# Kernel tuning notes

Hardware: AMD Instinct MI355X
Metric: run time of the kernel (lower is better)

The kernel has to match this reference:

```python
import jax, jax.numpy as jnp
import numpy as np

EMBED_DIM = 1024
NUM_HEADS = 16
HEAD_DIM = EMBED_DIM // NUM_HEADS


def setup_inputs() -> dict:
    key = jax.random.key(0)
    ks = jax.random.split(key, 9)
    B, S, D = 4, 2048, EMBED_DIM
    scale = 1.0 / np.sqrt(D)
    inp = {
        "x": jax.random.normal(ks[0], (B, S, D), dtype=jnp.float32),
        "wq": jax.random.normal(ks[1], (D, D), dtype=jnp.float32) * scale,
        "bq": jnp.zeros((D,), dtype=jnp.float32),
        "wk": jax.random.normal(ks[2], (D, D), dtype=jnp.float32) * scale,
        "bk": jnp.zeros((D,), dtype=jnp.float32),
        "wv": jax.random.normal(ks[3], (D, D), dtype=jnp.float32) * scale,
        "bv": jnp.zeros((D,), dtype=jnp.float32),
        "wo": jax.random.normal(ks[4], (D, D), dtype=jnp.float32) * scale,
        "bo": jnp.zeros((D,), dtype=jnp.float32),
    }
    return inp


def reference(x, wq, bq, wk, bk, wv, bv, wo, bo):
    B, S, D = x.shape
    H, Hd = NUM_HEADS, HEAD_DIM

    def split_heads(t):
        # [B, S, D] -> [B, H, S, Hd]
        return t.reshape(B, S, H, Hd).transpose(0, 2, 1, 3)

    q = split_heads(x @ wq.T + bq)
    k = split_heads(x @ wk.T + bk)
    v = split_heads(x @ wv.T + bv)

    scores = jnp.einsum("bhqd,bhkd->bhqk", q, k) / jnp.sqrt(jnp.float32(Hd))
    attn = jax.nn.softmax(scores, axis=-1)
    out = jnp.einsum("bhqk,bhkd->bhqd", attn, v)  # [B, H, S, Hd]
    out = out.transpose(0, 2, 1, 3).reshape(B, S, D)
    return out @ wo.T + bo
```

## Files before the change

### kernel.cpp

```cpp
#include <hip/hip_runtime.h>
#include <hip/hip_bf16.h>
#include <hip/hip_fp16.h>

typedef _Float16 f16;
typedef f16 f16x8 __attribute__((ext_vector_type(8)));
typedef f16 f16x4 __attribute__((ext_vector_type(4)));
typedef f16 f16x2 __attribute__((ext_vector_type(2)));
typedef float f32x4 __attribute__((ext_vector_type(4)));
typedef float f32x16 __attribute__((ext_vector_type(16)));
typedef unsigned int u32x4 __attribute__((ext_vector_type(4)));
typedef unsigned int u32x2 __attribute__((ext_vector_type(2)));

#define MFMA16(a, b, c) __builtin_amdgcn_mfma_f32_16x16x32_f16(a, b, c, 0, 0, 0)
#define MFMA32(a, b, c) __builtin_amdgcn_mfma_f32_32x32x16_f16(a, b, c, 0, 0, 0)

constexpr int BB = 4, SS = 2048, DD = 1024, HH = 16, HDIM = 64;
constexpr int MM = BB * SS;
constexpr float QSCALE = 0.125f * 1.44269504088896340736f;

__device__ __forceinline__ void gl_lds16(const void* g, void* l) {
  __builtin_amdgcn_global_load_lds((const __attribute__((address_space(1))) void*)g,
                                   (__attribute__((address_space(3))) void*)l, 16, 0, 0);
}

__global__ __launch_bounds__(256) void cvt_kernel(const float* __restrict__ in,
                                                  f16* __restrict__ out, int n4) {
  int i = blockIdx.x * 256 + threadIdx.x;
  if (i < n4) {
    f32x4 v = reinterpret_cast<const f32x4*>(in)[i];
    f16x4 o;
    o[0] = (f16)v[0]; o[1] = (f16)v[1]; o[2] = (f16)v[2]; o[3] = (f16)v[3];
    reinterpret_cast<f16x4*>(out)[i] = o;
  }
}

__global__ __launch_bounds__(256) void cvt4_kernel(const float* __restrict__ w0,
                                                   const float* __restrict__ w1,
                                                   const float* __restrict__ w2,
                                                   const float* __restrict__ w3,
                                                   f16* o0, f16* o1, f16* o2, f16* o3) {
  int i = blockIdx.x * 256 + threadIdx.x;
  const float* in; f16* out;
  switch (blockIdx.y) {
    case 0: in = w0; out = o0; break;
    case 1: in = w1; out = o1; break;
    case 2: in = w2; out = o2; break;
    default: in = w3; out = o3; break;
  }
  f32x4 v = reinterpret_cast<const f32x4*>(in)[i];
  f16x4 o;
  o[0] = (f16)v[0]; o[1] = (f16)v[1]; o[2] = (f16)v[2]; o[3] = (f16)v[3];
  reinterpret_cast<f16x4*>(out)[i] = o;
}

__device__ __forceinline__ int swz(int row, int slot) {
  return row * 64 + ((slot ^ (row & 7)) << 3);
}

__global__ __launch_bounds__(256) void qkv_kernel(const f16* __restrict__ A,
                                                  const f16* __restrict__ Wq,
                                                  const f16* __restrict__ Wk,
                                                  const f16* __restrict__ Wv,
                                                  const float* __restrict__ bq,
                                                  const float* __restrict__ bk,
                                                  const float* __restrict__ bv,
                                                  f16* __restrict__ Qo,
                                                  f16* __restrict__ Ko,
                                                  f16* __restrict__ Vo) {
  constexpr int K = 1024;
  __shared__ __align__(16) char smem_raw[128 * 136 * 2];
  f16* As = (f16*)smem_raw;
  f16* Ws = As + 128 * 64;

  const int mat = blockIdx.x >> 3;
  const f16* W = mat == 0 ? Wq : (mat == 1 ? Wk : Wv);
  const float* bias = mat == 0 ? bq : (mat == 1 ? bk : bv);
  const float scale = mat == 0 ? QSCALE : 1.0f;

  const int tid = threadIdx.x;
  const int m0 = blockIdx.y * 128, n0 = (blockIdx.x & 7) * 128;
  const int w = tid >> 6, lane = tid & 63;
  const int wm = (w >> 1) * 64, wn = (w & 1) * 64;
  const int g = lane >> 4, r = lane & 15;
  const int srow = lane >> 3;
  const int sslot = (lane & 7) ^ srow;

  f32x4 acc[4][4] = {};

  for (int k0 = 0; k0 < K; k0 += 64) {
#pragma unroll
    for (int i = 0; i < 4; ++i) {
      int rbase = w * 32 + i * 8;
      gl_lds16(A + (size_t)(m0 + rbase + srow) * K + k0 + sslot * 8, As + rbase * 64);
      gl_lds16(W + (size_t)(n0 + rbase + srow) * K + k0 + sslot * 8, Ws + rbase * 64);
    }
    __syncthreads();

#pragma unroll
    for (int ks = 0; ks < 2; ++ks) {
      f16x8 af[4], bf[4];
#pragma unroll
      for (int i = 0; i < 4; ++i) {
        af[i] = *reinterpret_cast<const f16x8*>(As + swz(wm + i * 16 + r, (ks << 2) | g));
        bf[i] = *reinterpret_cast<const f16x8*>(Ws + swz(wn + i * 16 + r, (ks << 2) | g));
      }
#pragma unroll
      for (int i = 0; i < 4; ++i)
#pragma unroll
        for (int j = 0; j < 4; ++j)
          acc[i][j] = MFMA16(af[i], bf[j], acc[i][j]);
    }
    __syncthreads();
  }

  if (mat < 2) {
    f16* o = mat == 0 ? Qo : Ko;
#pragma unroll
    for (int i = 0; i < 4; ++i)
#pragma unroll
      for (int j = 0; j < 4; ++j)
#pragma unroll
        for (int q = 0; q < 4; ++q) {
          int gm = m0 + wm + i * 16 + g * 4 + q;
          int gn = n0 + wn + j * 16 + r;
          float v = (acc[i][j][q] + bias[gn]) * scale;
          int b = gm >> 11, s = gm & 2047;
          int h = gn >> 6, hd = gn & 63;
          o[(((size_t)(b * HH + h)) * SS + s) * HDIM + hd] = (f16)v;
        }
  } else {
    __syncthreads();
    f16* T = (f16*)smem_raw;
#pragma unroll
    for (int i = 0; i < 4; ++i)
#pragma unroll
      for (int j = 0; j < 4; ++j)
#pragma unroll
        for (int q = 0; q < 4; ++q) {
          int ml = wm + i * 16 + g * 4 + q;
          int nl = wn + j * 16 + r;
          T[nl * 136 + ml] = (f16)(acc[i][j][q] + bias[n0 + nl]);
        }
    __syncthreads();
    const int b = m0 >> 11, sbase = m0 & 2047;
#pragma unroll
    for (int it = 0; it < 8; ++it) {
      int slot = it * 256 + tid;
      int nl = slot >> 4, mc = (slot & 15) * 8;
      u32x4 v = *reinterpret_cast<const u32x4*>(T + nl * 136 + mc);
      int gn = n0 + nl;
      int h = gn >> 6, hd = gn & 63;
      size_t addr = ((size_t)((b * HH + h) * HDIM + hd)) * SS + sbase + mc;
      *reinterpret_cast<u32x4*>(Vo + addr) = v;
    }
  }
}

__global__ __launch_bounds__(256) void oproj_kernel(const f16* __restrict__ A,
                                                    const f16* __restrict__ W,
                                                    const float* __restrict__ bias,
                                                    float* __restrict__ Out) {
  constexpr int K = 1024, N = 1024;
  __shared__ __align__(16) f16 As[128 * 64];
  __shared__ __align__(16) f16 Ws[128 * 64];

  const int tid = threadIdx.x;
  const int m0 = blockIdx.y * 128, n0 = blockIdx.x * 128;
  const int w = tid >> 6, lane = tid & 63;
  const int wm = (w >> 1) * 64, wn = (w & 1) * 64;
  const int g = lane >> 4, r = lane & 15;
  const int srow = lane >> 3;
  const int sslot = (lane & 7) ^ srow;

  f32x4 acc[4][4] = {};

  for (int k0 = 0; k0 < K; k0 += 64) {
#pragma unroll
    for (int i = 0; i < 4; ++i) {
      int rbase = w * 32 + i * 8;
      gl_lds16(A + (size_t)(m0 + rbase + srow) * K + k0 + sslot * 8, As + rbase * 64);
      gl_lds16(W + (size_t)(n0 + rbase + srow) * K + k0 + sslot * 8, Ws + rbase * 64);
    }
    __syncthreads();

#pragma unroll
    for (int ks = 0; ks < 2; ++ks) {
      f16x8 af[4], bf[4];
#pragma unroll
      for (int i = 0; i < 4; ++i) {
        af[i] = *reinterpret_cast<const f16x8*>(As + swz(wm + i * 16 + r, (ks << 2) | g));
        bf[i] = *reinterpret_cast<const f16x8*>(Ws + swz(wn + i * 16 + r, (ks << 2) | g));
      }
#pragma unroll
      for (int i = 0; i < 4; ++i)
#pragma unroll
        for (int j = 0; j < 4; ++j)
          acc[i][j] = MFMA16(af[i], bf[j], acc[i][j]);
    }
    __syncthreads();
  }

#pragma unroll
  for (int i = 0; i < 4; ++i)
#pragma unroll
    for (int j = 0; j < 4; ++j)
#pragma unroll
      for (int q = 0; q < 4; ++q) {
        int gm = m0 + wm + i * 16 + g * 4 + q;
        int gn = n0 + wn + j * 16 + r;
        Out[(size_t)gm * N + gn] = acc[i][j][q] + bias[gn];
      }
}

__global__ __launch_bounds__(256, 4) void attn_kernel(const f16* __restrict__ Q,
                                                      const f16* __restrict__ K,
                                                      const f16* __restrict__ Vt,
                                                      f16* __restrict__ AO) {
  __shared__ __align__(16) f16 Kls[2][64 * 64];
  __shared__ __align__(16) f16 Vls[2][64 * 64];
  __shared__ __align__(16) float Lw[4][32];

  const int tid = threadIdx.x;
  const int w = tid >> 6, lane = tid & 63;
  const int q31 = lane & 31;
  const int h = lane >> 5;
  const int bh = blockIdx.y;
  const int q0 = blockIdx.x * 128;
  const int srow = lane >> 3;
  const int sslot = (lane & 7) ^ srow;

  const f16* Kg = K + (size_t)bh * SS * HDIM;
  const f16* Vg = Vt + (size_t)bh * HDIM * SS;

  const f16* Qg = Q + ((size_t)bh * SS + q0 + w * 32 + q31) * HDIM + 8 * h;
  f16x8 qf[4];
#pragma unroll
  for (int m = 0; m < 4; ++m)
    qf[m] = *reinterpret_cast<const f16x8*>(Qg + 16 * m);

  f32x16 oacc[2] = {};
  float lsum = 0.f;

#pragma unroll
  for (int i = 0; i < 2; ++i) {
    int rbase = w * 16 + i * 8;
    gl_lds16(Kg + (size_t)(rbase + srow) * HDIM + sslot * 8, &Kls[0][rbase * 64]);
    gl_lds16(Vg + (size_t)(rbase + srow) * SS + sslot * 8, &Vls[0][rbase * 64]);
  }
  __syncthreads();

  for (int t = 0; t < SS / 64; ++t) {
    const int cur = t & 1;
    if (t < SS / 64 - 1) {
      const int kt = (t + 1) * 64;
#pragma unroll
      for (int i = 0; i < 2; ++i) {
        int rbase = w * 16 + i * 8;
        gl_lds16(Kg + (size_t)(kt + rbase + srow) * HDIM + sslot * 8, &Kls[cur ^ 1][rbase * 64]);
        gl_lds16(Vg + (size_t)(rbase + srow) * SS + kt + sslot * 8, &Vls[cur ^ 1][rbase * 64]);
      }
    }
    const f16* Kc = &Kls[cur][0];
    const f16* Vc = &Vls[cur][0];

#pragma unroll
    for (int kb = 0; kb < 2; ++kb) {
      f32x16 sacc = {};
      __builtin_amdgcn_s_setprio(1);
#pragma unroll
      for (int m = 0; m < 4; ++m) {
        f16x8 kf = *reinterpret_cast<const f16x8*>(Kc + swz(32 * kb + q31, 2 * m + h));
        sacc = MFMA32(kf, qf[m], sacc);
      }
      __builtin_amdgcn_s_setprio(0);

      unsigned pk[8];
#pragma unroll
      for (int rp = 0; rp < 4; ++rp)
#pragma unroll
        for (int p = 0; p < 2; ++p) {
          float e0 = __builtin_amdgcn_exp2f(sacc[4 * rp + 2 * p]);
          float e1 = __builtin_amdgcn_exp2f(sacc[4 * rp + 2 * p + 1]);
          pk[2 * rp + p] = __builtin_bit_cast(unsigned, __builtin_amdgcn_cvt_pkrtz(e0, e1));
        }

      f16x2 s01 = __builtin_bit_cast(f16x2, pk[0]) + __builtin_bit_cast(f16x2, pk[1]);
      f16x2 s23 = __builtin_bit_cast(f16x2, pk[2]) + __builtin_bit_cast(f16x2, pk[3]);
      f16x2 s45 = __builtin_bit_cast(f16x2, pk[4]) + __builtin_bit_cast(f16x2, pk[5]);
      f16x2 s67 = __builtin_bit_cast(f16x2, pk[6]) + __builtin_bit_cast(f16x2, pk[7]);
      f16x2 st = (s01 + s23) + (s45 + s67);
      lsum += (float)st[0] + (float)st[1];

#pragma unroll
      for (int jl = 0; jl < 2; ++jl) {
        auto s0 = __builtin_amdgcn_permlane32_swap(pk[4 * jl + 0], pk[4 * jl + 2], false, false);
        auto s1 = __builtin_amdgcn_permlane32_swap(pk[4 * jl + 1], pk[4 * jl + 3], false, false);
        u32x4 fw = {(unsigned)s0[0], (unsigned)s1[0], (unsigned)s0[1], (unsigned)s1[1]};
        f16x8 pa = __builtin_bit_cast(f16x8, fw);
        const int j = 2 * kb + jl;
        __builtin_amdgcn_s_setprio(1);
#pragma unroll
        for (int vb = 0; vb < 2; ++vb) {
          f16x8 vbf = *reinterpret_cast<const f16x8*>(Vc + swz(32 * vb + q31, 2 * j + h));
          oacc[vb] = MFMA32(pa, vbf, oacc[vb]);
        }
        __builtin_amdgcn_s_setprio(0);
      }
    }
    __syncthreads();
  }

  lsum += __shfl_xor(lsum, 32, 64);
  if (h == 0) Lw[w][q31] = 1.0f / lsum;

  f32x4 li[4];
#pragma unroll
  for (int rq = 0; rq < 4; ++rq)
    li[rq] = *reinterpret_cast<const f32x4*>(&Lw[w][8 * rq + 4 * h]);

  const int b = bh >> 4, head = bh & 15;
  f16* aobase = AO + ((size_t)(b * SS + q0 + 32 * w)) * DD + head * 64 + q31;
#pragma unroll
  for (int vb = 0; vb < 2; ++vb)
#pragma unroll
    for (int reg = 0; reg < 16; ++reg) {
      int q = (reg & 3) + 8 * (reg >> 2) + 4 * h;
      aobase[(size_t)q * DD + 32 * vb] = (f16)(oacc[vb][reg] * li[reg >> 2][reg & 3]);
    }
}

extern "C" void kernel_launch(void* const* d_in, const int* in_sizes, int n_in,
                              void* d_out, int out_size, void* d_ws, size_t ws_size,
                              hipStream_t stream) {
  (void)in_sizes; (void)n_in; (void)out_size; (void)ws_size;
  const float* x  = (const float*)d_in[0];
  const float* wq = (const float*)d_in[1];
  const float* bq = (const float*)d_in[2];
  const float* wk = (const float*)d_in[3];
  const float* bk = (const float*)d_in[4];
  const float* wv = (const float*)d_in[5];
  const float* bv = (const float*)d_in[6];
  const float* wo = (const float*)d_in[7];
  const float* bo = (const float*)d_in[8];
  float* out = (float*)d_out;

  char* ws = (char*)d_ws;
  f16* xh  = (f16*)ws; ws += (size_t)MM * DD * 2;
  f16* wqh = (f16*)ws; ws += (size_t)DD * DD * 2;
  f16* wkh = (f16*)ws; ws += (size_t)DD * DD * 2;
  f16* wvh = (f16*)ws; ws += (size_t)DD * DD * 2;
  f16* woh = (f16*)ws; ws += (size_t)DD * DD * 2;
  f16* Qb  = (f16*)ws; ws += (size_t)MM * DD * 2;
  f16* Kb  = (f16*)ws; ws += (size_t)MM * DD * 2;
  f16* Vtb = (f16*)ws; ws += (size_t)MM * DD * 2;
  f16* AOb = (f16*)ws; ws += (size_t)MM * DD * 2;

  cvt_kernel<<<MM * DD / 4 / 256, 256, 0, stream>>>(x, xh, MM * DD / 4);
  cvt4_kernel<<<dim3(DD * DD / 4 / 256, 4), 256, 0, stream>>>(wq, wk, wv, wo, wqh, wkh, wvh, woh);

  qkv_kernel<<<dim3(24, MM / 128), 256, 0, stream>>>(xh, wqh, wkh, wvh, bq, bk, bv, Qb, Kb, Vtb);

  attn_kernel<<<dim3(SS / 128, BB * HH), 256, 0, stream>>>(Qb, Kb, Vtb, AOb);

  oproj_kernel<<<dim3(DD / 128, MM / 128), 256, 0, stream>>>(AOb, woh, bo, out);
}
```

Before: 199.9 us.

## Pre-tile K and V in attention-friendly layout and merge conversion kernels

The QKV projection now writes K and V^T in a tiled layout of 64-row tiles with 8-element slot groups, so each attention tile is one contiguous block. The attention kernel can then load it with fully contiguous global-to-LDS copies and read fragments without swizzle arithmetic. The x and weight conversion kernels are also merged into one launch. The K epilogue now does scalar stores to a scattered layout, and the LDS reads depend on the new layout avoiding bank conflicts.

```diff
diff --git a/kernel.cpp b/kernel.cpp
--- a/kernel.cpp
+++ b/kernel.cpp
@@ -18,39 +18,34 @@
 constexpr int MM = BB * SS;
 constexpr float QSCALE = 0.125f * 1.44269504088896340736f;
 
+
 __device__ __forceinline__ void gl_lds16(const void* g, void* l) {
   __builtin_amdgcn_global_load_lds((const __attribute__((address_space(1))) void*)g,
                                    (__attribute__((address_space(3))) void*)l, 16, 0, 0);
 }
 
-__global__ __launch_bounds__(256) void cvt_kernel(const float* __restrict__ in,
-                                                  f16* __restrict__ out, int n4) {
-  int i = blockIdx.x * 256 + threadIdx.x;
-  if (i < n4) {
-    f32x4 v = reinterpret_cast<const f32x4*>(in)[i];
-    f16x4 o;
-    o[0] = (f16)v[0]; o[1] = (f16)v[1]; o[2] = (f16)v[2]; o[3] = (f16)v[3];
-    reinterpret_cast<f16x4*>(out)[i] = o;
-  }
-}
-
-__global__ __launch_bounds__(256) void cvt4_kernel(const float* __restrict__ w0,
-                                                   const float* __restrict__ w1,
-                                                   const float* __restrict__ w2,
-                                                   const float* __restrict__ w3,
-                                                   f16* o0, f16* o1, f16* o2, f16* o3) {
-  int i = blockIdx.x * 256 + threadIdx.x;
-  const float* in; f16* out;
-  switch (blockIdx.y) {
-    case 0: in = w0; out = o0; break;
-    case 1: in = w1; out = o1; break;
-    case 2: in = w2; out = o2; break;
-    default: in = w3; out = o3; break;
-  }
-  f32x4 v = reinterpret_cast<const f32x4*>(in)[i];
+__global__ __launch_bounds__(256) void cvt_all_kernel(const float* __restrict__ x,
+                                                      const float* __restrict__ w0,
+                                                      const float* __restrict__ w1,
+                                                      const float* __restrict__ w2,
+                                                      const float* __restrict__ w3,
+                                                      f16* xh, f16* o0, f16* o1,
+                                                      f16* o2, f16* o3) {
+  int bid = blockIdx.x;
+  const float* in; f16* out; int idx;
+  if (bid < MM * DD / 4 / 256) {
+    in = x; out = xh; idx = bid * 256 + threadIdx.x;
+  } else {
+    int wb = bid - MM * DD / 4 / 256;
+    int which = wb >> 10;
+    in = which == 0 ? w0 : which == 1 ? w1 : which == 2 ? w2 : w3;
+    out = which == 0 ? o0 : which == 1 ? o1 : which == 2 ? o2 : o3;
+    idx = (wb & 1023) * 256 + threadIdx.x;
+  }
+  f32x4 v = reinterpret_cast<const f32x4*>(in)[idx];
   f16x4 o;
   o[0] = (f16)v[0]; o[1] = (f16)v[1]; o[2] = (f16)v[2]; o[3] = (f16)v[3];
-  reinterpret_cast<f16x4*>(out)[i] = o;
+  reinterpret_cast<f16x4*>(out)[idx] = o;
 }
 
 __device__ __forceinline__ int swz(int row, int slot) {
@@ -113,8 +108,7 @@
     __syncthreads();
   }
 
-  if (mat < 2) {
-    f16* o = mat == 0 ? Qo : Ko;
+  if (mat == 0) {
 #pragma unroll
     for (int i = 0; i < 4; ++i)
 #pragma unroll
@@ -126,7 +120,23 @@
           float v = (acc[i][j][q] + bias[gn]) * scale;
           int b = gm >> 11, s = gm & 2047;
           int h = gn >> 6, hd = gn & 63;
-          o[(((size_t)(b * HH + h)) * SS + s) * HDIM + hd] = (f16)v;
+          Qo[(((size_t)(b * HH + h)) * SS + s) * HDIM + hd] = (f16)v;
+        }
+  } else if (mat == 1) {
+#pragma unroll
+    for (int i = 0; i < 4; ++i)
+#pragma unroll
+      for (int j = 0; j < 4; ++j)
+#pragma unroll
+        for (int q = 0; q < 4; ++q) {
+          int gm = m0 + wm + i * 16 + g * 4 + q;
+          int gn = n0 + wn + j * 16 + r;
+          float v = acc[i][j][q] + bias[gn];
+          int b = gm >> 11, s = gm & 2047;
+          int h = gn >> 6, hd = gn & 63;
+          int tile = s >> 6, row = s & 63, slot = hd >> 3, w8 = hd & 7;
+          size_t off = ((((size_t)(b * HH + h) * 32 + tile) * 8 + slot) * 64 + row) * 8 + w8;
+          Ko[off] = (f16)v;
         }
   } else {
     __syncthreads();
@@ -145,13 +155,13 @@
     const int b = m0 >> 11, sbase = m0 & 2047;
 #pragma unroll
     for (int it = 0; it < 8; ++it) {
-      int slot = it * 256 + tid;
-      int nl = slot >> 4, mc = (slot & 15) * 8;
-      u32x4 v = *reinterpret_cast<const u32x4*>(T + nl * 136 + mc);
-      int gn = n0 + nl;
-      int h = gn >> 6, hd = gn & 63;
-      size_t addr = ((size_t)((b * HH + h) * HDIM + hd)) * SS + sbase + mc;
-      *reinterpret_cast<u32x4*>(Vo + addr) = v;
+      int cid = it * 256 + tid;
+      int hd_l = cid & 127, sl = (cid >> 7) & 7, tl = cid >> 10;
+      u32x4 v = *reinterpret_cast<const u32x4*>(T + hd_l * 136 + tl * 64 + sl * 8);
+      int gn = n0 + hd_l, h = gn >> 6, hd = gn & 63;
+      int tile = (sbase >> 6) + tl;
+      size_t off = ((((size_t)(b * HH + h) * 32 + tile) * 8 + sl) * 64 + hd) * 8;
+      *reinterpret_cast<u32x4*>(Vo + off) = v;
     }
   }
 }
@@ -216,8 +226,8 @@
                                                       const f16* __restrict__ K,
                                                       const f16* __restrict__ Vt,
                                                       f16* __restrict__ AO) {
-  __shared__ __align__(16) f16 Kls[2][64 * 64];
-  __shared__ __align__(16) f16 Vls[2][64 * 64];
+  __shared__ __align__(16) f16 Kls[2][8 * 512];
+  __shared__ __align__(16) f16 Vls[2][8 * 512];
   __shared__ __align__(16) float Lw[4][32];
 
   const int tid = threadIdx.x;
@@ -226,11 +236,11 @@
   const int h = lane >> 5;
   const int bh = blockIdx.y;
   const int q0 = blockIdx.x * 128;
-  const int srow = lane >> 3;
-  const int sslot = (lane & 7) ^ srow;
-
-  const f16* Kg = K + (size_t)bh * SS * HDIM;
-  const f16* Vg = Vt + (size_t)bh * HDIM * SS;
+
+  const f16* Kg = K + (size_t)bh * (SS * HDIM);
+  const f16* Vg = Vt + (size_t)bh * (SS * HDIM);
+  const int s0 = 2 * w;
+  const int rofs = h * 512 + q31 * 8;
 
   const f16* Qg = Q + ((size_t)bh * SS + q0 + w * 32 + q31) * HDIM + 8 * h;
   f16x8 qf[4];
@@ -243,21 +253,22 @@
 
 #pragma unroll
   for (int i = 0; i < 2; ++i) {
-    int rbase = w * 16 + i * 8;
-    gl_lds16(Kg + (size_t)(rbase + srow) * HDIM + sslot * 8, &Kls[0][rbase * 64]);
-    gl_lds16(Vg + (size_t)(rbase + srow) * SS + sslot * 8, &Vls[0][rbase * 64]);
+    int s_idx = s0 + i;
+    gl_lds16(Kg + (size_t)(s_idx * 64 + lane) * 8, &Kls[0][s_idx * 512]);
+    gl_lds16(Vg + (size_t)(s_idx * 64 + lane) * 8, &Vls[0][s_idx * 512]);
   }
   __syncthreads();
 
   for (int t = 0; t < SS / 64; ++t) {
     const int cur = t & 1;
     if (t < SS / 64 - 1) {
-      const int kt = (t + 1) * 64;
 #pragma unroll
       for (int i = 0; i < 2; ++i) {
-        int rbase = w * 16 + i * 8;
-        gl_lds16(Kg + (size_t)(kt + rbase + srow) * HDIM + sslot * 8, &Kls[cur ^ 1][rbase * 64]);
-        gl_lds16(Vg + (size_t)(rbase + srow) * SS + kt + sslot * 8, &Vls[cur ^ 1][rbase * 64]);
+        int s_idx = s0 + i;
+        gl_lds16(Kg + (size_t)((t + 1) * 512 + s_idx * 64 + lane) * 8,
+                 &Kls[cur ^ 1][s_idx * 512]);
+        gl_lds16(Vg + (size_t)((t + 1) * 512 + s_idx * 64 + lane) * 8,
+                 &Vls[cur ^ 1][s_idx * 512]);
       }
     }
     const f16* Kc = &Kls[cur][0];
@@ -269,7 +280,7 @@
       __builtin_amdgcn_s_setprio(1);
 #pragma unroll
       for (int m = 0; m < 4; ++m) {
-        f16x8 kf = *reinterpret_cast<const f16x8*>(Kc + swz(32 * kb + q31, 2 * m + h));
+        f16x8 kf = *reinterpret_cast<const f16x8*>(Kc + m * 1024 + kb * 256 + rofs);
         sacc = MFMA32(kf, qf[m], sacc);
       }
       __builtin_amdgcn_s_setprio(0);
@@ -293,15 +304,15 @@
 
 #pragma unroll
       for (int jl = 0; jl < 2; ++jl) {
-        auto s0 = __builtin_amdgcn_permlane32_swap(pk[4 * jl + 0], pk[4 * jl + 2], false, false);
-        auto s1 = __builtin_amdgcn_permlane32_swap(pk[4 * jl + 1], pk[4 * jl + 3], false, false);
-        u32x4 fw = {(unsigned)s0[0], (unsigned)s1[0], (unsigned)s0[1], (unsigned)s1[1]};
+        auto sw0 = __builtin_amdgcn_permlane32_swap(pk[4 * jl + 0], pk[4 * jl + 2], false, false);
+        auto sw1 = __builtin_amdgcn_permlane32_swap(pk[4 * jl + 1], pk[4 * jl + 3], false, false);
+        u32x4 fw = {(unsigned)sw0[0], (unsigned)sw1[0], (unsigned)sw0[1], (unsigned)sw1[1]};
         f16x8 pa = __builtin_bit_cast(f16x8, fw);
         const int j = 2 * kb + jl;
         __builtin_amdgcn_s_setprio(1);
 #pragma unroll
         for (int vb = 0; vb < 2; ++vb) {
-          f16x8 vbf = *reinterpret_cast<const f16x8*>(Vc + swz(32 * vb + q31, 2 * j + h));
+          f16x8 vbf = *reinterpret_cast<const f16x8*>(Vc + j * 1024 + vb * 256 + rofs);
           oacc[vb] = MFMA32(pa, vbf, oacc[vb]);
         }
         __builtin_amdgcn_s_setprio(0);
@@ -355,8 +366,8 @@
   f16* Vtb = (f16*)ws; ws += (size_t)MM * DD * 2;
   f16* AOb = (f16*)ws; ws += (size_t)MM * DD * 2;
 
-  cvt_kernel<<<MM * DD / 4 / 256, 256, 0, stream>>>(x, xh, MM * DD / 4);
-  cvt4_kernel<<<dim3(DD * DD / 4 / 256, 4), 256, 0, stream>>>(wq, wk, wv, wo, wqh, wkh, wvh, woh);
+  cvt_all_kernel<<<MM * DD / 4 / 256 + 4 * (DD * DD / 4 / 256), 256, 0, stream>>>(
+      x, wq, wk, wv, wo, xh, wqh, wkh, wvh, woh);
 
   qkv_kernel<<<dim3(24, MM / 128), 256, 0, stream>>>(xh, wqh, wkh, wvh, bq, bk, bv, Qb, Kb, Vtb);
 
```

New measurement: 197.1 us. Within noise of the previous version (-1.4%).
